# Kernel optimization log

Measured on AMD Instinct MI355X. Metric: run time of the kernel, lower is better.

Reference implementation:

```python
import jax, jax.numpy as jnp
import numpy as np

B = 64
H_FS = W_FS = 56
IN_DIM, OUT_DIM, NUM_HEADS = 96, 192, 2
HEAD_DIM = OUT_DIM // NUM_HEADS  # 96
STRIDE_Q, STRIDE_KV = (2, 2), (4, 4)
REL_RANGE = 2 * (H_FS // STRIDE_Q[0]) - 1  # 55
LN_EPS = 1e-5


def setup_inputs() -> dict:
    key = jax.random.key(0)
    ks = jax.random.split(key, 12)
    N = H_FS * W_FS + 1  # +1 cls token
    s = 0.02
    d = {
        "hidden_states": jax.random.normal(ks[0], (B, N, IN_DIM), jnp.float32),
        "Wq": jax.random.normal(ks[1], (IN_DIM, OUT_DIM), jnp.float32) * s,
        "bq": jnp.zeros((OUT_DIM,), jnp.float32),
        "Wk": jax.random.normal(ks[2], (IN_DIM, OUT_DIM), jnp.float32) * s,
        "bk": jnp.zeros((OUT_DIM,), jnp.float32),
        "Wv": jax.random.normal(ks[3], (IN_DIM, OUT_DIM), jnp.float32) * s,
        "bv": jnp.zeros((OUT_DIM,), jnp.float32),
        # depthwise pool convs: (C_out=C, C_in/groups=1, kh, kw)
        "pool_q_w": jax.random.normal(ks[4], (IN_DIM, 1, 3, 3), jnp.float32) * 0.1,
        "pool_k_w": jax.random.normal(ks[5], (IN_DIM, 1, 3, 3), jnp.float32) * 0.1,
        "pool_v_w": jax.random.normal(ks[6], (IN_DIM, 1, 3, 3), jnp.float32) * 0.1,
        "gq": jnp.ones((IN_DIM,), jnp.float32), "betaq": jnp.zeros((IN_DIM,), jnp.float32),
        "gk": jnp.ones((IN_DIM,), jnp.float32), "betak": jnp.zeros((IN_DIM,), jnp.float32),
        "gv": jnp.ones((IN_DIM,), jnp.float32), "betav": jnp.zeros((IN_DIM,), jnp.float32),
        "rel_h": jax.random.normal(ks[7], (REL_RANGE, HEAD_DIM), jnp.float32) * s,
        "rel_w": jax.random.normal(ks[8], (REL_RANGE, HEAD_DIM), jnp.float32) * s,
        "height": H_FS,
        "width": W_FS,
    }
    return d


def _layernorm(x, g, b):
    m = x.mean(-1, keepdims=True)
    v = ((x - m) ** 2).mean(-1, keepdims=True)
    return (x - m) * jax.lax.rsqrt(v + LN_EPS) * g + b


def _pool(x, w, stride, g, b, height, width):
    # x: (B, folds=1, N, C) with cls token first
    bsz, _, _, C = x.shape
    cls_tok, rest = x[:, :, :1], x[:, :, 1:]
    sp = rest.reshape(bsz, height, width, C).transpose(0, 3, 1, 2)  # (B, C, H, W)
    y = jax.lax.conv_general_dilated(
        sp, w, stride, [(1, 1), (1, 1)], feature_group_count=C,
        dimension_numbers=("NCHW", "OIHW", "NCHW"))
    hp, wp = y.shape[2], y.shape[3]
    y = y.reshape(bsz, 1, C, hp * wp).transpose(0, 1, 3, 2)  # (B, 1, N', C)
    y = jnp.concatenate([cls_tok, y], axis=2)
    return _layernorm(y, g, b), (hp, wp)


def _rel_idx(qn, kn):
    q_ratio = max(kn / qn, 1.0)
    k_ratio = max(qn / kn, 1.0)
    dist = (np.arange(qn)[:, None] * q_ratio - np.arange(kn)[None, :] * k_ratio
            + (kn - 1) * k_ratio)
    return dist.astype(np.int64)


def reference(hidden_states, Wq, bq, Wk, bk, Wv, bv, pool_q_w, pool_k_w, pool_v_w,
              gq, betaq, gk, betak, gv, betav, rel_h, rel_w, height, width):
    bsz, N, C = hidden_states.shape
    h = hidden_states.reshape(bsz, N, 1, C).transpose(0, 2, 1, 3)  # (B, folds=1, N, C)

    q, (qh, qw) = _pool(h, pool_q_w, STRIDE_Q, gq, betaq, height, width)
    k, (kh, kw) = _pool(h, pool_k_w, STRIDE_KV, gk, betak, height, width)
    v, _ = _pool(h, pool_v_w, STRIDE_KV, gv, betav, height, width)

    def proj(x, W, bias, n):
        x = x.transpose(0, 2, 1, 3).reshape(bsz, n, -1)
        x = x @ W + bias
        return x.reshape(bsz, n, NUM_HEADS, HEAD_DIM).transpose(0, 2, 1, 3)

    nq, nk = qh * qw + 1, kh * kw + 1
    q = proj(q, Wq, bq, nq)  # (B, H, nq, d)
    k = proj(k, Wk, bk, nk)
    v = proj(v, Wv, bv, nk)

    scale = HEAD_DIM ** -0.5
    attn = jnp.einsum("bhqd,bhkd->bhqk", q * scale, k)

    # decomposed spatial relative positional bias (cls offset = 1)
    Rh = rel_h[_rel_idx(qh, kh)]  # (qh, kh, d)
    Rw = rel_w[_rel_idx(qw, kw)]  # (qw, kw, d)
    rq = q[:, :, 1:].reshape(bsz, NUM_HEADS, qh, qw, HEAD_DIM)
    eh = jnp.einsum("byhwc,hkc->byhwk", rq, Rh)
    ew = jnp.einsum("byhwc,wkc->byhwk", rq, Rw)
    blk = (attn[:, :, 1:, 1:].reshape(bsz, NUM_HEADS, qh, qw, kh, kw)
           + eh[..., :, None] + ew[..., None, :])
    attn = attn.at[:, :, 1:, 1:].set(blk.reshape(bsz, NUM_HEADS, qh * qw, kh * kw))

    attn = jax.nn.softmax(attn, axis=-1)
    out = jnp.einsum("bhqk,bhkd->bhqd", attn, v)
    out = out.at[:, :, 1:].add(q[:, :, 1:])  # residual pooling (skip cls)
    return out.transpose(0, 2, 1, 3).reshape(bsz, nq, OUT_DIM)
```

## Files before the change

### kernel.cpp

```cpp
#include <hip/hip_runtime.h>
#include <hip/hip_bf16.h>
#include <hip/hip_fp16.h>

#define B_    64
#define HFS   56
#define CIN   96
#define NQ    785
#define NK    197
#define QW    28
#define KW    14
#define NTOT  3137
#define NQP   800
#define NKP   208
#define NKPV  224
#define VROWS 112
#define KSCL  0.10206207261596575f

typedef __attribute__((ext_vector_type(8))) short short8;
typedef __attribute__((ext_vector_type(4))) short shortx4;
typedef __attribute__((ext_vector_type(4))) float floatx4;

__device__ __forceinline__ short f2s(float x) {
    __hip_bfloat16 h = __float2bfloat16(x);
    return *reinterpret_cast<short*>(&h);
}
__device__ __forceinline__ float s2f(short s) {
    __hip_bfloat16 h; *reinterpret_cast<short*>(&h) = s;
    return __bfloat162float(h);
}
__device__ __forceinline__ short8 ld8(const short* p) {
    return *reinterpret_cast<const short8*>(p);
}
__device__ __forceinline__ unsigned pkbf(float a, float b) {
    return (unsigned)(unsigned short)f2s(a) | ((unsigned)(unsigned short)f2s(b) << 16);
}
__device__ __forceinline__ unsigned pkhf(float a, float b) {
    __half2 h = __floats2half2_rn(a, b);
    return *reinterpret_cast<unsigned*>(&h);
}
__device__ __forceinline__ float hflo(unsigned w) {
    __half2 h = *reinterpret_cast<__half2*>(&w);
    return __half2float(__low2half(h));
}
__device__ __forceinline__ float hfhi(unsigned w) {
    __half2 h = *reinterpret_cast<__half2*>(&w);
    return __half2float(__high2half(h));
}

#define MFMA16(a,b,c) __builtin_amdgcn_mfma_f32_16x16x32_bf16((a),(b),(c),0,0,0)

__global__ void prep_kernel(const float* __restrict__ Wq, const float* __restrict__ Wk,
                            const float* __restrict__ Wv, const float* __restrict__ relh,
                            const float* __restrict__ relw,
                            const float* __restrict__ pqw, const float* __restrict__ pkw,
                            const float* __restrict__ pvw,
                            short* __restrict__ WTq, short* __restrict__ WTk,
                            short* __restrict__ WTv, short* __restrict__ relc,
                            short* __restrict__ vt,
                            float* __restrict__ cwqT, float* __restrict__ cwkT,
                            float* __restrict__ cwvT)
{
    int i = blockIdx.x * 256 + threadIdx.x;
    if (i < 18432)      { int o = i/96, c = i%96;              WTq[o*96+c] = f2s(Wq[c*192+o]); }
    else if (i < 36864) { int j = i-18432; int o=j/96,c=j%96;  WTk[o*96+c] = f2s(Wk[c*192+o]*KSCL); }
    else if (i < 55296) { int j = i-36864; int o=j/96,c=j%96;  WTv[o*96+c] = f2s(Wv[c*192+o]); }
    else if (i < 66048) {
        int j = i - 55296;  int r = j/96, c = j%96;
        float v = (r < 54) ? relh[r*96+c] : ((r < 108) ? relw[(r-54)*96+c] : 0.f);
        relc[r*96+c] = f2s(v);
    } else if (i < 721408) {
        int j2 = i - 66048;
        int bh = j2 / 5120, r = j2 % 5120;
        int row, tok; short val;
        if (r < 3584) { row = 96 + r/224; tok = r%224;
                        val = (row == 96 && tok < NK) ? (short)0x3F80 : (short)0; }
        else          { int rr = r-3584; row = rr/16; tok = 208 + (rr%16); val = 0; }
        vt[((long)bh*VROWS + row)*NKPV + tok] = val;
    } else if (i < 724000) {
        int j = i - 721408;
        int w = j / 864, r = j % 864;
        int c = r / 9, off = r % 9;
        const float* src = (w == 0) ? pqw : (w == 1) ? pkw : pvw;
        float*       dst = (w == 0) ? cwqT : (w == 1) ? cwkT : cwvT;
        dst[off*96 + c] = src[c*9 + off];
    }
}

__device__ __forceinline__ void red16_2(float& s, float& ss) {
    #pragma unroll
    for (int off = 8; off >= 1; off >>= 1) {
        s  += __shfl_xor(s,  off, 16);
        ss += __shfl_xor(ss, off, 16);
    }
}

__device__ __forceinline__ void ln6_store(const float* x, float m, float r,
    const float* __restrict__ g, const float* __restrict__ beta,
    int c0, short* __restrict__ outp)
{
    float2 g0 = *reinterpret_cast<const float2*>(g + c0);
    float2 g1 = *reinterpret_cast<const float2*>(g + c0 + 2);
    float2 g2 = *reinterpret_cast<const float2*>(g + c0 + 4);
    float2 b0 = *reinterpret_cast<const float2*>(beta + c0);
    float2 b1 = *reinterpret_cast<const float2*>(beta + c0 + 2);
    float2 b2 = *reinterpret_cast<const float2*>(beta + c0 + 4);
    unsigned o0 = pkbf((x[0]-m)*r*g0.x + b0.x, (x[1]-m)*r*g0.y + b0.y);
    unsigned o1 = pkbf((x[2]-m)*r*g1.x + b1.x, (x[3]-m)*r*g1.y + b1.y);
    unsigned o2 = pkbf((x[4]-m)*r*g2.x + b2.x, (x[5]-m)*r*g2.y + b2.y);
    *reinterpret_cast<unsigned*>(outp)     = o0;
    *reinterpret_cast<unsigned*>(outp + 2) = o1;
    *reinterpret_cast<unsigned*>(outp + 4) = o2;
}

__device__ __forceinline__ void zero6(short* __restrict__ outp) {
    *reinterpret_cast<unsigned*>(outp)     = 0u;
    *reinterpret_cast<unsigned*>(outp + 2) = 0u;
    *reinterpret_cast<unsigned*>(outp + 4) = 0u;
}

__global__ __launch_bounds__(256) void pool_ln_kernel(
    const float* __restrict__ hs,
    const float* __restrict__ cwqT, const float* __restrict__ cwkT, const float* __restrict__ cwvT,
    const float* __restrict__ gq, const float* __restrict__ betaq,
    const float* __restrict__ gk, const float* __restrict__ betak,
    const float* __restrict__ gv, const float* __restrict__ betav,
    short* __restrict__ pq, short* __restrict__ pk, short* __restrict__ pv)
{
    const int wid  = threadIdx.x >> 6;
    const int lane = threadIdx.x & 63;
    const int sub  = lane >> 4;
    const int li   = lane & 15;
    const int c0   = li * 6;
    const int gid  = blockIdx.x * 4 + wid;
    const int b    = gid / 252;
    const int slot = gid % 252;
    const long hb  = (long)b * NTOT * CIN;

    if (slot < 200) {
        int t = slot*4 + sub;
        short* outp = pq + ((long)b*NQP + t)*CIN + c0;
        if (t >= NQ) { zero6(outp); return; }
        float x[6];
        #pragma unroll
        for (int i = 0; i < 6; ++i) x[i] = 0.f;
        if (t == 0) {
            const float* hp = hs + hb + c0;
            float2 a0 = *reinterpret_cast<const float2*>(hp);
            float2 a1 = *reinterpret_cast<const float2*>(hp + 2);
            float2 a2 = *reinterpret_cast<const float2*>(hp + 4);
            x[0]=a0.x; x[1]=a0.y; x[2]=a1.x; x[3]=a1.y; x[4]=a2.x; x[5]=a2.y;
        } else {
            int j = t - 1, oy = j / QW, ox = j % QW;
            #pragma unroll
            for (int dy = 0; dy < 3; ++dy) {
                int iy = oy*2 - 1 + dy;
                #pragma unroll
                for (int dx = 0; dx < 3; ++dx) {
                    int ix = ox*2 - 1 + dx;
                    if (iy >= 0 && iy < HFS && ix >= 0 && ix < HFS) {
                        const float* hp = hs + hb + (long)(1 + iy*HFS + ix)*CIN + c0;
                        const float* wp = cwqT + (dy*3+dx)*96 + c0;
                        float2 h0 = *reinterpret_cast<const float2*>(hp);
                        float2 h1 = *reinterpret_cast<const float2*>(hp + 2);
                        float2 h2 = *reinterpret_cast<const float2*>(hp + 4);
                        float2 w0 = *reinterpret_cast<const float2*>(wp);
                        float2 w1 = *reinterpret_cast<const float2*>(wp + 2);
                        float2 w2 = *reinterpret_cast<const float2*>(wp + 4);
                        x[0] = fmaf(h0.x, w0.x, x[0]); x[1] = fmaf(h0.y, w0.y, x[1]);
                        x[2] = fmaf(h1.x, w1.x, x[2]); x[3] = fmaf(h1.y, w1.y, x[3]);
                        x[4] = fmaf(h2.x, w2.x, x[4]); x[5] = fmaf(h2.y, w2.y, x[5]);
                    }
                }
            }
        }
        float s  = (x[0]+x[1]) + (x[2]+x[3]) + (x[4]+x[5]);
        float ss = fmaf(x[0],x[0], fmaf(x[1],x[1], fmaf(x[2],x[2],
                   fmaf(x[3],x[3], fmaf(x[4],x[4], x[5]*x[5])))));
        red16_2(s, ss);
        float m   = s * (1.f/96.f);
        float var = ss * (1.f/96.f) - m*m;
        float r   = rsqrtf(var + 1e-5f);
        ln6_store(x, m, r, gq, betaq, c0, outp);
    } else {
        int tok = (slot - 200)*4 + sub;
        short* ok_ = pk + ((long)b*NKP + tok)*CIN + c0;
        short* ov_ = pv + ((long)b*NKP + tok)*CIN + c0;
        if (tok >= NK) { zero6(ok_); zero6(ov_); return; }
        float xk[6], xv[6];
        #pragma unroll
        for (int i = 0; i < 6; ++i) { xk[i] = 0.f; xv[i] = 0.f; }
        if (tok == 0) {
            const float* hp = hs + hb + c0;
            float2 a0 = *reinterpret_cast<const float2*>(hp);
            float2 a1 = *reinterpret_cast<const float2*>(hp + 2);
            float2 a2 = *reinterpret_cast<const float2*>(hp + 4);
            xk[0]=xv[0]=a0.x; xk[1]=xv[1]=a0.y; xk[2]=xv[2]=a1.x;
            xk[3]=xv[3]=a1.y; xk[4]=xv[4]=a2.x; xk[5]=xv[5]=a2.y;
        } else {
            int j = tok - 1, oy = j / KW, ox = j % KW;
            #pragma unroll
            for (int dy = 0; dy < 3; ++dy) {
                int iy = oy*4 - 1 + dy;
                #pragma unroll
                for (int dx = 0; dx < 3; ++dx) {
                    int ix = ox*4 - 1 + dx;
                    if (iy >= 0 && iy < HFS && ix >= 0 && ix < HFS) {
                        const float* hp = hs + hb + (long)(1 + iy*HFS + ix)*CIN + c0;
                        int wo = (dy*3+dx)*96 + c0;
                        float2 h0 = *reinterpret_cast<const float2*>(hp);
                        float2 h1 = *reinterpret_cast<const float2*>(hp + 2);
                        float2 h2 = *reinterpret_cast<const float2*>(hp + 4);
                        float2 k0 = *reinterpret_cast<const float2*>(cwkT + wo);
                        float2 k1 = *reinterpret_cast<const float2*>(cwkT + wo + 2);
                        float2 k2 = *reinterpret_cast<const float2*>(cwkT + wo + 4);
                        float2 v0 = *reinterpret_cast<const float2*>(cwvT + wo);
                        float2 v1 = *reinterpret_cast<const float2*>(cwvT + wo + 2);
                        float2 v2 = *reinterpret_cast<const float2*>(cwvT + wo + 4);
                        xk[0] = fmaf(h0.x, k0.x, xk[0]); xk[1] = fmaf(h0.y, k0.y, xk[1]);
                        xk[2] = fmaf(h1.x, k1.x, xk[2]); xk[3] = fmaf(h1.y, k1.y, xk[3]);
                        xk[4] = fmaf(h2.x, k2.x, xk[4]); xk[5] = fmaf(h2.y, k2.y, xk[5]);
                        xv[0] = fmaf(h0.x, v0.x, xv[0]); xv[1] = fmaf(h0.y, v0.y, xv[1]);
                        xv[2] = fmaf(h1.x, v1.x, xv[2]); xv[3] = fmaf(h1.y, v1.y, xv[3]);
                        xv[4] = fmaf(h2.x, v2.x, xv[4]); xv[5] = fmaf(h2.y, v2.y, xv[5]);
                    }
                }
            }
        }
        float sk  = (xk[0]+xk[1]) + (xk[2]+xk[3]) + (xk[4]+xk[5]);
        float ssk = fmaf(xk[0],xk[0], fmaf(xk[1],xk[1], fmaf(xk[2],xk[2],
                    fmaf(xk[3],xk[3], fmaf(xk[4],xk[4], xk[5]*xk[5])))));
        float sv  = (xv[0]+xv[1]) + (xv[2]+xv[3]) + (xv[4]+xv[5]);
        float ssv = fmaf(xv[0],xv[0], fmaf(xv[1],xv[1], fmaf(xv[2],xv[2],
                    fmaf(xv[3],xv[3], fmaf(xv[4],xv[4], xv[5]*xv[5])))));
        red16_2(sk, ssk);
        red16_2(sv, ssv);
        float mk = sk * (1.f/96.f), vark = ssk * (1.f/96.f) - mk*mk;
        float mv = sv * (1.f/96.f), varv = ssv * (1.f/96.f) - mv*mv;
        float rk = rsqrtf(vark + 1e-5f);
        float rv = rsqrtf(varv + 1e-5f);
        ln6_store(xk, mk, rk, gk, betak, c0, ok_);
        ln6_store(xv, mv, rv, gv, betav, c0, ov_);
    }
}

__global__ __launch_bounds__(256) void proj_mfma_kernel(
    const short* __restrict__ pq, const short* __restrict__ pk, const short* __restrict__ pv,
    const short* __restrict__ WTq, const short* __restrict__ WTk, const short* __restrict__ WTv,
    const float* __restrict__ bq, const float* __restrict__ bk, const float* __restrict__ bv,
    short* __restrict__ qb, short* __restrict__ kb, short* __restrict__ vt)
{
    int wid  = threadIdx.x >> 6;
    int lane = threadIdx.x & 63;
    int quad = lane >> 4, col = lane & 15;
    int wt = blockIdx.x * 4 + wid;

    if (wt < 2016) {
        const short *A, *WT; const float* bias; short* outp;
        int ntokp, row0; float bsc;
        if (wt < 1600) { A = pq; WT = WTq; bias = bq; outp = qb; ntokp = NQP; row0 = wt*32; bsc = 1.f; }
        else           { A = pk; WT = WTk; bias = bk; outp = kb; ntokp = NKP; row0 = (wt-1600)*32; bsc = KSCL; }

        short8 bt[2][3];
        #pragma unroll
        for (int ti = 0; ti < 2; ++ti)
            #pragma unroll
            for (int cc = 0; cc < 3; ++cc)
                bt[ti][cc] = ld8(A + (long)(row0 + ti*16 + col)*96 + cc*32 + quad*8);

        int bT[2], tokT[2];
        #pragma unroll
        for (int ti = 0; ti < 2; ++ti) {
            int r = row0 + ti*16;
            bT[ti] = r / ntokp;
            tokT[ti] = (r % ntokp) + col;
        }

        #pragma unroll
        for (int nt = 0; nt < 12; ++nt) {
            short8 af[3];
            #pragma unroll
            for (int cc = 0; cc < 3; ++cc)
                af[cc] = ld8(WT + (nt*16 + col)*96 + cc*32 + quad*8);
            int o0 = nt*16 + quad*4;
            float4 bo = *reinterpret_cast<const float4*>(bias + o0);
            int h  = (o0 >= 96) ? 1 : 0;
            int d0 = o0 - h*96;
            #pragma unroll
            for (int ti = 0; ti < 2; ++ti) {
                floatx4 acc = {0.f, 0.f, 0.f, 0.f};
                #pragma unroll
                for (int cc = 0; cc < 3; ++cc)
                    acc = MFMA16(af[cc], bt[ti][cc], acc);
                shortx4 val;
                val.x = f2s(acc[0] + bo.x*bsc);
                val.y = f2s(acc[1] + bo.y*bsc);
                val.z = f2s(acc[2] + bo.z*bsc);
                val.w = f2s(acc[3] + bo.w*bsc);
                *reinterpret_cast<shortx4*>(outp + ((long)(bT[ti]*2 + h)*ntokp + tokT[ti])*96 + d0) = val;
            }
        }
    } else {
        int row0 = (wt - 2016) * 32;
        short8 at[2][3];
        #pragma unroll
        for (int ti = 0; ti < 2; ++ti)
            #pragma unroll
            for (int cc = 0; cc < 3; ++cc)
                at[ti][cc] = ld8(pv + (long)(row0 + ti*16 + col)*96 + cc*32 + quad*8);

        int bT[2], t0T[2];
        #pragma unroll
        for (int ti = 0; ti < 2; ++ti) {
            int r = row0 + ti*16;
            bT[ti] = r / NKP;
            t0T[ti] = (r % NKP) + quad*4;
        }

        #pragma unroll
        for (int nt = 0; nt < 12; ++nt) {
            short8 bf[3];
            #pragma unroll
            for (int cc = 0; cc < 3; ++cc)
                bf[cc] = ld8(WTv + (nt*16 + col)*96 + cc*32 + quad*8);
            int o = nt*16 + col;
            int h = (o >= 96) ? 1 : 0;
            int d = o - h*96;
            float bo = bv[o];
            #pragma unroll
            for (int ti = 0; ti < 2; ++ti) {
                floatx4 acc = {0.f, 0.f, 0.f, 0.f};
                #pragma unroll
                for (int cc = 0; cc < 3; ++cc)
                    acc = MFMA16(at[ti][cc], bf[cc], acc);
                shortx4 val;
                val.x = (t0T[ti]+0 < NK) ? f2s(acc[0] + bo) : (short)0;
                val.y = (t0T[ti]+1 < NK) ? f2s(acc[1] + bo) : (short)0;
                val.z = (t0T[ti]+2 < NK) ? f2s(acc[2] + bo) : (short)0;
                val.w = (t0T[ti]+3 < NK) ? f2s(acc[3] + bo) : (short)0;
                *reinterpret_cast<shortx4*>(vt + ((long)(bT[ti]*2 + h)*VROWS + d)*NKPV + t0T[ti]) = val;
            }
        }
    }
}

__global__ __launch_bounds__(256) void attn_kernel(
    const short* __restrict__ qb, const short* __restrict__ kb,
    const short* __restrict__ vt, const short* __restrict__ relc,
    float* __restrict__ out)
{
    __shared__ __align__(16) short smem[8][16][232];

    int tid  = threadIdx.x;
    int wid  = tid >> 6;
    int lane = tid & 63;
    int quad = lane >> 4, col = lane & 15;

    int bid = blockIdx.x;
    int tb  = (bid & 7) * 100 + (bid >> 3);
    int wt  = tb * 4 + wid;
    int bh  = wt / 25;
    int tp  = wt % 25;
    int q0  = tp * 32;

    const short* qrow = qb + ((long)bh*NQP + q0)*96;
    short8 aq[2][3];
    #pragma unroll
    for (int ti = 0; ti < 2; ++ti)
        #pragma unroll
        for (int c = 0; c < 3; ++c)
            aq[ti][c] = ld8(qrow + (ti*16 + col)*96 + c*32 + quad*8);

    #pragma unroll
    for (int rt = 0; rt < 7; ++rt) {
        short8 bf[3];
        #pragma unroll
        for (int c = 0; c < 3; ++c)
            bf[c] = ld8(relc + (rt*16 + col)*96 + c*32 + quad*8);
        #pragma unroll
        for (int ti = 0; ti < 2; ++ti) {
            floatx4 acc = {0.f, 0.f, 0.f, 0.f};
            #pragma unroll
            for (int c = 0; c < 3; ++c)
                acc = MFMA16(aq[ti][c], bf[c], acc);
            #pragma unroll
            for (int reg = 0; reg < 4; ++reg)
                smem[wid*2+ti][quad*4 + reg][rt*16 + col] = f2s(acc[reg]);
        }
    }

    int qyo[2][4], qxo[2][4];
    #pragma unroll
    for (int ti = 0; ti < 2; ++ti)
        #pragma unroll
        for (int reg = 0; reg < 4; ++reg) {
            int qq = q0 + ti*16 + quad*4 + reg;
            int jj = (qq > 0) ? (qq - 1) : 0;
            qyo[ti][reg] = jj / QW;
            qxo[ti][reg] = jj % QW;
        }

    unsigned bpk[2][13][2];
    #pragma unroll
    for (int kt = 0; kt < 13; ++kt) {
        int k  = kt*16 + col;
        int kk = (k > 0) ? (k - 1) : 0;
        int ky = kk / 14;  ky = (ky < 13) ? ky : 13;
        int kx = kk - 14*ky;
        int oh  = 26 - 2*ky;
        int ow2 = 26 - 2*kx;
        #pragma unroll
        for (int ti = 0; ti < 2; ++ti) {
            float bs[4];
            #pragma unroll
            for (int reg = 0; reg < 4; ++reg) {
                const short* er = &smem[wid*2+ti][quad*4 + reg][0];
                float bias = s2f(er[qyo[ti][reg] + oh]) + s2f(er[54 + qxo[ti][reg] + ow2]);
                if (kt == 0) bias = (col == 0) ? 0.f : bias;
                if (q0 == 0 && ti == 0 && reg == 0) bias = (quad == 0) ? 0.f : bias;
                bs[reg] = bias;
            }
            bpk[ti][kt][0] = pkhf(bs[0], bs[1]);
            bpk[ti][kt][1] = pkhf(bs[2], bs[3]);
        }
    }

    const short* kbase = kb + (long)bh*NKP*96;
    #pragma unroll
    for (int kt = 0; kt < 13; ++kt) {
        short8 bf[3];
        #pragma unroll
        for (int c = 0; c < 3; ++c)
            bf[c] = ld8(kbase + (kt*16 + col)*96 + c*32 + quad*8);
        int k = kt*16 + col;
        #pragma unroll
        for (int ti = 0; ti < 2; ++ti) {
            floatx4 acc = {0.f, 0.f, 0.f, 0.f};
            #pragma unroll
            for (int c = 0; c < 3; ++c)
                acc = MFMA16(aq[ti][c], bf[c], acc);
            unsigned w0 = bpk[ti][kt][0], w1 = bpk[ti][kt][1];
            smem[wid*2+ti][quad*4 + 0][k] = f2s(__expf(acc[0] + hflo(w0)));
            smem[wid*2+ti][quad*4 + 1][k] = f2s(__expf(acc[1] + hfhi(w0)));
            smem[wid*2+ti][quad*4 + 2][k] = f2s(__expf(acc[2] + hflo(w1)));
            smem[wid*2+ti][quad*4 + 3][k] = f2s(__expf(acc[3] + hfhi(w1)));
        }
    }
    #pragma unroll
    for (int ti = 0; ti < 2; ++ti)
        #pragma unroll
        for (int reg = 0; reg < 4; ++reg)
            smem[wid*2+ti][quad*4 + reg][208 + col] = 0;

    floatx4 o[2][7];
    #pragma unroll
    for (int ti = 0; ti < 2; ++ti)
        #pragma unroll
        for (int nt = 0; nt < 7; ++nt) o[ti][nt] = floatx4{0.f, 0.f, 0.f, 0.f};
    const short* vbase = vt + (long)bh*VROWS*NKPV;
    #pragma unroll
    for (int c = 0; c < 7; ++c) {
        short8 apA = ld8(&smem[wid*2+0][col][c*32 + quad*8]);
        short8 apB = ld8(&smem[wid*2+1][col][c*32 + quad*8]);
        #pragma unroll
        for (int nt = 0; nt < 7; ++nt) {
            short8 bf = ld8(vbase + (nt*16 + col)*NKPV + c*32 + quad*8);
            o[0][nt] = MFMA16(apA, bf, o[0][nt]);
            o[1][nt] = MFMA16(apB, bf, o[1][nt]);
        }
    }

    float inv[2][4];
    #pragma unroll
    for (int ti = 0; ti < 2; ++ti)
        #pragma unroll
        for (int reg = 0; reg < 4; ++reg) {
            float srow = __shfl(o[ti][6][reg], lane & 48, 64);
            inv[ti][reg] = 1.0f / srow;
        }
    int b = bh >> 1, h = bh & 1;
    #pragma unroll
    for (int ti = 0; ti < 2; ++ti)
        #pragma unroll
        for (int nt = 0; nt < 6; ++nt) {
            int ch = nt*16 + col;
            #pragma unroll
            for (int reg = 0; reg < 4; ++reg) {
                int q = q0 + ti*16 + quad*4 + reg;
                if (q < NQ) {
                    float val = o[ti][nt][reg] * inv[ti][reg];
                    if (q > 0) val += s2f(qb[((long)bh*NQP + q)*96 + ch]);
                    out[((long)b*NQ + q)*192 + h*96 + ch] = val;
                }
            }
        }
}

extern "C" void kernel_launch(void* const* d_in, const int* in_sizes, int n_in,
                              void* d_out, int out_size, void* d_ws, size_t ws_size,
                              hipStream_t stream)
{
    const float* hs    = (const float*)d_in[0];
    const float* Wq    = (const float*)d_in[1];
    const float* bq    = (const float*)d_in[2];
    const float* Wk    = (const float*)d_in[3];
    const float* bk    = (const float*)d_in[4];
    const float* Wv    = (const float*)d_in[5];
    const float* bv    = (const float*)d_in[6];
    const float* pqw   = (const float*)d_in[7];
    const float* pkw   = (const float*)d_in[8];
    const float* pvw   = (const float*)d_in[9];
    const float* gq    = (const float*)d_in[10];
    const float* betaq = (const float*)d_in[11];
    const float* gk    = (const float*)d_in[12];
    const float* betak = (const float*)d_in[13];
    const float* gv    = (const float*)d_in[14];
    const float* betav = (const float*)d_in[15];
    const float* relh  = (const float*)d_in[16];
    const float* relw  = (const float*)d_in[17];
    float* out = (float*)d_out;

    short* pq   = (short*)d_ws;
    short* pk   = pq  + (long)B_*NQP*CIN;
    short* pv   = pk  + (long)B_*NKP*CIN;
    short* qb   = pv  + (long)B_*NKP*CIN;
    short* kb   = qb  + (long)128*NQP*96;
    short* vt   = kb  + (long)128*NKP*96;
    short* WTq  = vt  + (long)128*VROWS*NKPV;
    short* WTk  = WTq + 192*96;
    short* WTv  = WTk + 192*96;
    short* relc = WTv + 192*96;
    float* cwqT = (float*)(relc + 112*96);
    float* cwkT = cwqT + 9*96;
    float* cwvT = cwkT + 9*96;

    prep_kernel<<<2829, 256, 0, stream>>>(Wq, Wk, Wv, relh, relw,
                                          pqw, pkw, pvw,
                                          WTq, WTk, WTv, relc, vt,
                                          cwqT, cwkT, cwvT);

    pool_ln_kernel<<<(B_*1008)/16, 256, 0, stream>>>(
        hs, cwqT, cwkT, cwvT, gq, betaq, gk, betak, gv, betav, pq, pk, pv);

    proj_mfma_kernel<<<2432/4, 256, 0, stream>>>(
        pq, pk, pv, WTq, WTk, WTv, bq, bk, bv, qb, kb, vt);

    attn_kernel<<<800, 256, 0, stream>>>(qb, kb, vt, relc, out);
}
```

Before: 245.0 us.

## Use single-wave attention blocks, exp2 with log2e folding, and MFMA priority hints

```diff
diff --git a/kernel.cpp b/kernel.cpp
--- a/kernel.cpp
+++ b/kernel.cpp
@@ -15,6 +15,8 @@
 #define NKPV  224
 #define VROWS 112
 #define KSCL  0.10206207261596575f
+#define LOG2E 1.4426950408889634f
+#define KSCL2 (KSCL*LOG2E)
 
 typedef __attribute__((ext_vector_type(8))) short short8;
 typedef __attribute__((ext_vector_type(4))) short shortx4;
@@ -62,12 +64,12 @@
 {
     int i = blockIdx.x * 256 + threadIdx.x;
     if (i < 18432)      { int o = i/96, c = i%96;              WTq[o*96+c] = f2s(Wq[c*192+o]); }
-    else if (i < 36864) { int j = i-18432; int o=j/96,c=j%96;  WTk[o*96+c] = f2s(Wk[c*192+o]*KSCL); }
+    else if (i < 36864) { int j = i-18432; int o=j/96,c=j%96;  WTk[o*96+c] = f2s(Wk[c*192+o]*KSCL2); }
     else if (i < 55296) { int j = i-36864; int o=j/96,c=j%96;  WTv[o*96+c] = f2s(Wv[c*192+o]); }
     else if (i < 66048) {
         int j = i - 55296;  int r = j/96, c = j%96;
         float v = (r < 54) ? relh[r*96+c] : ((r < 108) ? relw[(r-54)*96+c] : 0.f);
-        relc[r*96+c] = f2s(v);
+        relc[r*96+c] = f2s(v*LOG2E);
     } else if (i < 721408) {
         int j2 = i - 66048;
         int bh = j2 / 5120, r = j2 % 5120;
@@ -258,7 +260,7 @@
         const short *A, *WT; const float* bias; short* outp;
         int ntokp, row0; float bsc;
         if (wt < 1600) { A = pq; WT = WTq; bias = bq; outp = qb; ntokp = NQP; row0 = wt*32; bsc = 1.f; }
-        else           { A = pk; WT = WTk; bias = bk; outp = kb; ntokp = NKP; row0 = (wt-1600)*32; bsc = KSCL; }
+        else           { A = pk; WT = WTk; bias = bk; outp = kb; ntokp = NKP; row0 = (wt-1600)*32; bsc = KSCL2; }
 
         short8 bt[2][3];
         #pragma unroll
@@ -343,21 +345,18 @@
     }
 }
 
-__global__ __launch_bounds__(256) void attn_kernel(
+__global__ __launch_bounds__(64, 2) void attn_kernel(
     const short* __restrict__ qb, const short* __restrict__ kb,
     const short* __restrict__ vt, const short* __restrict__ relc,
     float* __restrict__ out)
 {
-    __shared__ __align__(16) short smem[8][16][232];
-
-    int tid  = threadIdx.x;
-    int wid  = tid >> 6;
-    int lane = tid & 63;
+    __shared__ __align__(16) short smem[2][16][232];
+
+    int lane = threadIdx.x & 63;
     int quad = lane >> 4, col = lane & 15;
 
     int bid = blockIdx.x;
-    int tb  = (bid & 7) * 100 + (bid >> 3);
-    int wt  = tb * 4 + wid;
+    int wt  = (bid & 7) * 400 + (bid >> 3);
     int bh  = wt / 25;
     int tp  = wt % 25;
     int q0  = tp * 32;
@@ -384,7 +383,7 @@
                 acc = MFMA16(aq[ti][c], bf[c], acc);
             #pragma unroll
             for (int reg = 0; reg < 4; ++reg)
-                smem[wid*2+ti][quad*4 + reg][rt*16 + col] = f2s(acc[reg]);
+                smem[ti][quad*4 + reg][rt*16 + col] = f2s(acc[reg]);
         }
     }
 
@@ -413,7 +412,7 @@
             float bs[4];
             #pragma unroll
             for (int reg = 0; reg < 4; ++reg) {
-                const short* er = &smem[wid*2+ti][quad*4 + reg][0];
+                const short* er = &smem[ti][quad*4 + reg][0];
                 float bias = s2f(er[qyo[ti][reg] + oh]) + s2f(er[54 + qxo[ti][reg] + ow2]);
                 if (kt == 0) bias = (col == 0) ? 0.f : bias;
                 if (q0 == 0 && ti == 0 && reg == 0) bias = (quad == 0) ? 0.f : bias;
@@ -432,24 +431,31 @@
         for (int c = 0; c < 3; ++c)
             bf[c] = ld8(kbase + (kt*16 + col)*96 + c*32 + quad*8);
         int k = kt*16 + col;
-        #pragma unroll
-        for (int ti = 0; ti < 2; ++ti) {
-            floatx4 acc = {0.f, 0.f, 0.f, 0.f};
-            #pragma unroll
-            for (int c = 0; c < 3; ++c)
-                acc = MFMA16(aq[ti][c], bf[c], acc);
-            unsigned w0 = bpk[ti][kt][0], w1 = bpk[ti][kt][1];
-            smem[wid*2+ti][quad*4 + 0][k] = f2s(__expf(acc[0] + hflo(w0)));
-            smem[wid*2+ti][quad*4 + 1][k] = f2s(__expf(acc[1] + hfhi(w0)));
-            smem[wid*2+ti][quad*4 + 2][k] = f2s(__expf(acc[2] + hflo(w1)));
-            smem[wid*2+ti][quad*4 + 3][k] = f2s(__expf(acc[3] + hfhi(w1)));
-        }
+        __builtin_amdgcn_s_setprio(1);
+        floatx4 accA = {0.f, 0.f, 0.f, 0.f};
+        floatx4 accB = {0.f, 0.f, 0.f, 0.f};
+        #pragma unroll
+        for (int c = 0; c < 3; ++c) {
+            accA = MFMA16(aq[0][c], bf[c], accA);
+            accB = MFMA16(aq[1][c], bf[c], accB);
+        }
+        __builtin_amdgcn_s_setprio(0);
+        unsigned a0 = bpk[0][kt][0], a1 = bpk[0][kt][1];
+        unsigned b0 = bpk[1][kt][0], b1 = bpk[1][kt][1];
+        smem[0][quad*4 + 0][k] = f2s(__builtin_amdgcn_exp2f(accA[0] + hflo(a0)));
+        smem[0][quad*4 + 1][k] = f2s(__builtin_amdgcn_exp2f(accA[1] + hfhi(a0)));
+        smem[0][quad*4 + 2][k] = f2s(__builtin_amdgcn_exp2f(accA[2] + hflo(a1)));
+        smem[0][quad*4 + 3][k] = f2s(__builtin_amdgcn_exp2f(accA[3] + hfhi(a1)));
+        smem[1][quad*4 + 0][k] = f2s(__builtin_amdgcn_exp2f(accB[0] + hflo(b0)));
+        smem[1][quad*4 + 1][k] = f2s(__builtin_amdgcn_exp2f(accB[1] + hfhi(b0)));
+        smem[1][quad*4 + 2][k] = f2s(__builtin_amdgcn_exp2f(accB[2] + hflo(b1)));
+        smem[1][quad*4 + 3][k] = f2s(__builtin_amdgcn_exp2f(accB[3] + hfhi(b1)));
     }
     #pragma unroll
     for (int ti = 0; ti < 2; ++ti)
         #pragma unroll
         for (int reg = 0; reg < 4; ++reg)
-            smem[wid*2+ti][quad*4 + reg][208 + col] = 0;
+            smem[ti][quad*4 + reg][208 + col] = 0;
 
     floatx4 o[2][7];
     #pragma unroll
@@ -459,14 +465,19 @@
     const short* vbase = vt + (long)bh*VROWS*NKPV;
     #pragma unroll
     for (int c = 0; c < 7; ++c) {
-        short8 apA = ld8(&smem[wid*2+0][col][c*32 + quad*8]);
-        short8 apB = ld8(&smem[wid*2+1][col][c*32 + quad*8]);
+        short8 apA = ld8(&smem[0][col][c*32 + quad*8]);
+        short8 apB = ld8(&smem[1][col][c*32 + quad*8]);
+        short8 bf[7];
+        #pragma unroll
+        for (int nt = 0; nt < 7; ++nt)
+            bf[nt] = ld8(vbase + (nt*16 + col)*NKPV + c*32 + quad*8);
+        __builtin_amdgcn_s_setprio(1);
         #pragma unroll
         for (int nt = 0; nt < 7; ++nt) {
-            short8 bf = ld8(vbase + (nt*16 + col)*NKPV + c*32 + quad*8);
-            o[0][nt] = MFMA16(apA, bf, o[0][nt]);
-            o[1][nt] = MFMA16(apB, bf, o[1][nt]);
-        }
+            o[0][nt] = MFMA16(apA, bf[nt], o[0][nt]);
+            o[1][nt] = MFMA16(apB, bf[nt], o[1][nt]);
+        }
+        __builtin_amdgcn_s_setprio(0);
     }
 
     float inv[2][4];
@@ -544,5 +555,5 @@
     proj_mfma_kernel<<<2432/4, 256, 0, stream>>>(
         pq, pk, pv, WTq, WTk, WTv, bq, bk, bv, qb, kb, vt);
 
-    attn_kernel<<<800, 256, 0, stream>>>(qb, kb, vt, relc, out);
-}
+    attn_kernel<<<3200, 64, 0, stream>>>(qb, kb, vt, relc, out);
+}
```

Measured after the change: 244.1 us. Within noise of the previous version (-0.4%).
